# Performance work log

Measured on AMD Instinct MI355X. Metric: run time of the kernel, lower is better.

## Reference

```python
import jax, jax.numpy as jnp
import numpy as np

N_NODES = 50000
N_EDGES = 800000
F_NODE = 64
F_EDGE = 64
HIDDEN = 128


def setup_inputs() -> dict:
    key = jax.random.key(0)
    ks = jax.random.split(key, 12)
    glorot = lambda k, shape: jax.random.normal(k, shape, jnp.float32) * (2.0 / (shape[0] + shape[1])) ** 0.5
    return {
        "x": jax.random.normal(ks[0], (N_NODES, F_NODE), jnp.float32),
        "edge_index": jax.random.randint(ks[1], (2, N_EDGES), 0, N_NODES, jnp.int64),
        "edge_attr": jax.random.normal(ks[2], (N_EDGES, F_EDGE), jnp.float32),
        # edge model: MLP(concat(x_src, x_dst, edge_attr)) -> new edge_attr
        "We1": glorot(ks[3], (2 * F_NODE + F_EDGE, HIDDEN)),
        "be1": jnp.zeros((HIDDEN,), jnp.float32),
        "We2": glorot(ks[4], (HIDDEN, F_EDGE)),
        "be2": jnp.zeros((F_EDGE,), jnp.float32),
        # node model: MLP(concat(x, mean_{e: dst==i} edge_attr_e)) -> new x
        "Wn1": glorot(ks[5], (F_NODE + F_EDGE, HIDDEN)),
        "bn1": jnp.zeros((HIDDEN,), jnp.float32),
        "Wn2": glorot(ks[6], (HIDDEN, F_NODE)),
        "bn2": jnp.zeros((F_NODE,), jnp.float32),
    }


def _mlp(h, W1, b1, W2, b2):
    return jax.nn.relu(h @ W1 + b1) @ W2 + b2


def reference(x, edge_index, edge_attr, We1, be1, We2, be2, Wn1, bn1, Wn2, bn2):
    row, col = edge_index[0], edge_index[1]
    # edge model: message on each edge  [E, 2F+Fe] -> [E, Fe]
    edge_in = jnp.concatenate([x[row], x[col], edge_attr], axis=-1)
    edge_attr = _mlp(edge_in, We1, be1, We2, be2)
    # node model: mean-aggregate incoming messages at dst (col), then MLP
    agg = jax.ops.segment_sum(edge_attr, col, num_segments=N_NODES)
    cnt = jax.ops.segment_sum(jnp.ones((edge_attr.shape[0],), x.dtype), col, num_segments=N_NODES)
    agg = agg / jnp.maximum(cnt, 1.0)[:, None]
    node_in = jnp.concatenate([x, agg], axis=-1)
    x = _mlp(node_in, Wn1, bn1, Wn2, bn2)
    return (x, edge_attr)
```

## Files before the change

kernel.cpp:

```cpp
#include <hip/hip_runtime.h>


typedef __attribute__((ext_vector_type(8))) short bf16x8;
typedef __attribute__((ext_vector_type(4))) float f4;
typedef __attribute__((ext_vector_type(8))) unsigned short us8;

constexpr int NN  = 50000;
constexpr int NE  = 800000;
constexpr int FN  = 64;
constexpr int FE  = 64;
constexpr int HID = 128;
constexpr int K1  = 2 * FN + FE;
constexpr int K2  = FN + FE;
constexpr int GRID_E    = 2500;
constexpr int TPB_TILES = 5;
constexpr int ZAGG_TOT = NN * FE / 8;
constexpr int PACK_TOT = 7168;
constexpr int XCVT_TOT = NN * FN / 8;
constexpr int PREP_TOT = ZAGG_TOT + PACK_TOT + XCVT_TOT + NE;

__device__ __forceinline__ float b2f(unsigned short u) {
  union { unsigned int i; float f; } v; v.i = ((unsigned int)u) << 16; return v.f;
}
__device__ __forceinline__ unsigned short f2b(float f) {
  union { float f; unsigned int i; } v; v.f = f;
  unsigned int r = v.i + 0x7FFFu + ((v.i >> 16) & 1u);
  return (unsigned short)(r >> 16);
}
__device__ __forceinline__ void st16(const f4* r, unsigned short* dst) {
  us8 o0, o1;
#pragma unroll
  for (int j = 0; j < 4; j++) {
    o0[j] = f2b(r[0][j]); o0[4 + j] = f2b(r[1][j]);
    o1[j] = f2b(r[2][j]); o1[4 + j] = f2b(r[3][j]);
  }
  *(us8*)dst = o0; *(us8*)(dst + 8) = o1;
}
__device__ __forceinline__ void ld16(const float* p, f4* r) {
  const f4* pp = (const f4*)p;
  r[0] = pp[0]; r[1] = pp[1]; r[2] = pp[2]; r[3] = pp[3];
}
__device__ __forceinline__ f4 MF(bf16x8 a, bf16x8 b, f4 c) {
  return __builtin_amdgcn_mfma_f32_16x16x32_bf16(a, b, c, 0, 0, 0);
}
__device__ __forceinline__ void pk_atomic_add_bf16(unsigned short* addr, unsigned int data) {
  asm volatile("global_atomic_pk_add_bf16 %0, %1, off" :: "v"(addr), "v"(data) : "memory");
}

__global__ void zero_cnt_kernel(float* __restrict__ cnt) {
  int i = blockIdx.x * 256 + threadIdx.x;
  if (i < NN) cnt[i] = 0.f;
}

__global__ void prep_kernel(const float* __restrict__ We1, const float* __restrict__ We2,
                            const float* __restrict__ Wn1, const float* __restrict__ Wn2,
                            const float* __restrict__ x, const int* __restrict__ ei,
                            unsigned short* __restrict__ P, unsigned short* __restrict__ xb,
                            unsigned short* __restrict__ aggb, float* __restrict__ cnt) {
  int idx = blockIdx.x * 256 + threadIdx.x;
  if (idx < ZAGG_TOT) {
    *(us8*)(aggb + (size_t)idx * 8) = (us8)0;
  } else if (idx < ZAGG_TOT + PACK_TOT) {
    int w = idx - ZAGG_TOT;
    const float* W; unsigned short* Pd; int N;
    if (w < 3072)      { W = We1; Pd = P; N = HID; }
    else if (w < 4096) { W = We2; Pd = P + 24576; N = FE;  w -= 3072; }
    else if (w < 6144) { W = Wn1; Pd = P + 32768; N = HID; w -= 4096; }
    else               { W = Wn2; Pd = P + 49152; N = FN;  w -= 6144; }
    const int l  = w & 63;
    const int nt = (w >> 6) % (N >> 4);
    const int s  = w / ((N >> 4) << 6);
    const int col = nt * 16 + (l & 15);
    const int k0  = s * 32 + (l >> 4) * 8;
    us8 o;
#pragma unroll
    for (int j = 0; j < 8; j++) o[j] = f2b(W[(size_t)(k0 + j) * N + col]);
    *(us8*)(Pd + (size_t)w * 8) = o;
  } else if (idx < ZAGG_TOT + PACK_TOT + XCVT_TOT) {
    const int i = idx - ZAGG_TOT - PACK_TOT;
    const f4* p = (const f4*)(x + (size_t)i * 8);
    f4 a = p[0], b = p[1];
    us8 o;
#pragma unroll
    for (int j = 0; j < 4; j++) { o[j] = f2b(a[j]); o[4 + j] = f2b(b[j]); }
    *(us8*)(xb + (size_t)i * 8) = o;
  } else if (idx < PREP_TOT) {
    const int e = idx - ZAGG_TOT - PACK_TOT - XCVT_TOT;
    atomicAdd(&cnt[ei[NE + e]], 1.0f);
  }
}

__global__ __launch_bounds__(256) void edge_mlp(
    const unsigned short* __restrict__ xb, const int* __restrict__ ei,
    const float* __restrict__ ea,
    const unsigned short* __restrict__ P1, const float* __restrict__ be1,
    const unsigned short* __restrict__ P2, const float* __restrict__ be2,
    float* __restrict__ eout, unsigned short* __restrict__ aggb) {
  __shared__ unsigned short sA[2][64][200];
  __shared__ unsigned short sH[64][136];
  __shared__ int sC[2][64];
  const int tid  = threadIdx.x;
  const int wave = tid >> 6, lane = tid & 63;
  const int mrow = lane & 15, kq = lane >> 4;
  const int el = tid >> 2, q = tid & 3;

  us8 rx0[2], rx1[2];
  f4  rea[4];
  int rN, cN;
  int cStage;

  {
    const int ge = blockIdx.x * 64 + el;
    const int r = ei[ge], c = ei[NE + ge];
    cStage = c;
    const us8* pr = (const us8*)(xb + (size_t)r * FN + q * 16);
    rx0[0] = pr[0]; rx0[1] = pr[1];
    const us8* pc = (const us8*)(xb + (size_t)c * FN + q * 16);
    rx1[0] = pc[0]; rx1[1] = pc[1];
    ld16(ea + (size_t)ge * FE + q * 16, rea);
    const int ge1 = (blockIdx.x + GRID_E) * 64 + el;
    rN = ei[ge1];
    cN = ei[NE + ge1];
    sC[0][el] = cStage;
    *(us8*)&sA[0][el][q * 16]          = rx0[0];
    *(us8*)&sA[0][el][q * 16 + 8]      = rx0[1];
    *(us8*)&sA[0][el][64 + q * 16]     = rx1[0];
    *(us8*)&sA[0][el][64 + q * 16 + 8] = rx1[1];
    st16(rea, &sA[0][el][128 + q * 16]);
  }

  for (int j = 0; j < TPB_TILES; j++) {
    const int cur = j & 1, nxt = cur ^ 1;
    const int e0 = (blockIdx.x + j * GRID_E) * 64;
    __syncthreads();

    if (j + 1 < TPB_TILES) {
      const int rr = rN, cc = cN;
      cStage = cc;
      const int geN = e0 + GRID_E * 64 + el;
      const us8* pr = (const us8*)(xb + (size_t)rr * FN + q * 16);
      rx0[0] = pr[0]; rx0[1] = pr[1];
      const us8* pc = (const us8*)(xb + (size_t)cc * FN + q * 16);
      rx1[0] = pc[0]; rx1[1] = pc[1];
      ld16(ea + (size_t)geN * FE + q * 16, rea);
      if (j + 2 < TPB_TILES) {
        const int ge2 = e0 + 2 * GRID_E * 64 + el;
        rN = ei[ge2];
        cN = ei[NE + ge2];
      }
    }
    __builtin_amdgcn_sched_barrier(0);

    f4 acc[4][2];
#pragma unroll
    for (int m = 0; m < 4; m++) { acc[m][0] = (f4)0.f; acc[m][1] = (f4)0.f; }
    const int nt0 = wave * 2;
#pragma unroll
    for (int s = 0; s < 6; s++) {
      bf16x8 b0 = *(const bf16x8*)(P1 + (((size_t)s * 8 + nt0)     * 64 + lane) * 8);
      bf16x8 b1 = *(const bf16x8*)(P1 + (((size_t)s * 8 + nt0 + 1) * 64 + lane) * 8);
#pragma unroll
      for (int m = 0; m < 4; m++) {
        bf16x8 a = *(const bf16x8*)&sA[cur][m * 16 + mrow][s * 32 + kq * 8];
        acc[m][0] = MF(a, b0, acc[m][0]);
        acc[m][1] = MF(a, b1, acc[m][1]);
      }
    }

    {
      const int c0 = nt0 * 16 + mrow, c1 = c0 + 16;
      const float bb0 = be1[c0], bb1 = be1[c1];
      const int rb = kq * 4;
#pragma unroll
      for (int m = 0; m < 4; m++)
#pragma unroll
        for (int i = 0; i < 4; i++) {
          sH[m * 16 + rb + i][c0] = f2b(fmaxf(acc[m][0][i] + bb0, 0.f));
          sH[m * 16 + rb + i][c1] = f2b(fmaxf(acc[m][1][i] + bb1, 0.f));
        }
    }
    __syncthreads();

    f4 a2[4];
#pragma unroll
    for (int m = 0; m < 4; m++) a2[m] = (f4)0.f;
#pragma unroll
    for (int s = 0; s < 4; s++) {
      bf16x8 b = *(const bf16x8*)(P2 + (((size_t)s * 4 + wave) * 64 + lane) * 8);
#pragma unroll
      for (int m = 0; m < 4; m++) {
        bf16x8 a = *(const bf16x8*)&sH[m * 16 + mrow][s * 32 + kq * 8];
        a2[m] = MF(a, b, a2[m]);
      }
    }

    {
      const int col = wave * 16 + mrow;
      const float bb = be2[col];
      const int rb = kq * 4;
      const bool even = ((lane & 1) == 0);
#pragma unroll
      for (int m = 0; m < 4; m++)
#pragma unroll
        for (int i = 0; i < 4; i++) {
          const int er = m * 16 + rb + i;
          const float v = a2[m][i] + bb;
          eout[(size_t)(e0 + er) * FE + col] = v;
          const float vp = __shfl_xor(v, 1);
          if (even) {
            const unsigned int pk =
                (unsigned int)f2b(v) | ((unsigned int)f2b(vp) << 16);
            pk_atomic_add_bf16(aggb + ((size_t)sC[cur][er] * FE + col), pk);
          }
        }
    }

    if (j + 1 < TPB_TILES) {
      sC[nxt][el] = cStage;
      *(us8*)&sA[nxt][el][q * 16]          = rx0[0];
      *(us8*)&sA[nxt][el][q * 16 + 8]      = rx0[1];
      *(us8*)&sA[nxt][el][64 + q * 16]     = rx1[0];
      *(us8*)&sA[nxt][el][64 + q * 16 + 8] = rx1[1];
      st16(rea, &sA[nxt][el][128 + q * 16]);
    }
  }
}

__global__ __launch_bounds__(256) void node_mlp(
    const unsigned short* __restrict__ xb, const unsigned short* __restrict__ aggb,
    const float* __restrict__ cnt,
    const unsigned short* __restrict__ P1, const float* __restrict__ bn1,
    const unsigned short* __restrict__ P2, const float* __restrict__ bn2,
    float* __restrict__ xout) {
  __shared__ unsigned short sA[32][136];
  unsigned short (*sH)[136] = (unsigned short(*)[136])&sA[0][0];
  const int tid = threadIdx.x;
  const int n0  = blockIdx.x * 32;

  {
    const int nl = tid >> 3, q = tid & 7;
    const int gn = n0 + nl;
    if (gn < NN) {
      if (q < 4) {
        const us8* p = (const us8*)(xb + (size_t)gn * FN + q * 16);
        *(us8*)&sA[nl][q * 16]     = p[0];
        *(us8*)&sA[nl][q * 16 + 8] = p[1];
      } else {
        const float inv = 1.0f / fmaxf(cnt[gn], 1.0f);
        const int q4 = q - 4;
        const us8* pa = (const us8*)(aggb + (size_t)gn * FE + q4 * 16);
#pragma unroll
        for (int seg = 0; seg < 2; seg++) {
          us8 a = pa[seg];
          us8 o;
#pragma unroll
          for (int jj = 0; jj < 8; jj++) o[jj] = f2b(b2f(a[jj]) * inv);
          *(us8*)&sA[nl][64 + q4 * 16 + seg * 8] = o;
        }
      }
    } else {
      us8 z = (us8)0;
      *(us8*)&sA[nl][(q & 3) * 16]     = z;
      *(us8*)&sA[nl][(q & 3) * 16 + 8] = z;
      *(us8*)&sA[nl][64 + (q & 3) * 16]     = z;
      *(us8*)&sA[nl][64 + (q & 3) * 16 + 8] = z;
    }
  }
  __syncthreads();

  const int wave = tid >> 6, lane = tid & 63;
  const int mrow = lane & 15, kq = lane >> 4;

  f4 acc[2][2];
#pragma unroll
  for (int m = 0; m < 2; m++) { acc[m][0] = (f4)0.f; acc[m][1] = (f4)0.f; }
  const int nt0 = wave * 2;
#pragma unroll
  for (int s = 0; s < 4; s++) {
    bf16x8 b0 = *(const bf16x8*)(P1 + (((size_t)s * 8 + nt0)     * 64 + lane) * 8);
    bf16x8 b1 = *(const bf16x8*)(P1 + (((size_t)s * 8 + nt0 + 1) * 64 + lane) * 8);
#pragma unroll
    for (int m = 0; m < 2; m++) {
      bf16x8 a = *(const bf16x8*)&sA[m * 16 + mrow][s * 32 + kq * 8];
      acc[m][0] = MF(a, b0, acc[m][0]);
      acc[m][1] = MF(a, b1, acc[m][1]);
    }
  }
  __syncthreads();

  {
    const int c0 = nt0 * 16 + mrow, c1 = c0 + 16;
    const float bb0 = bn1[c0], bb1 = bn1[c1];
    const int rb = kq * 4;
#pragma unroll
    for (int m = 0; m < 2; m++)
#pragma unroll
      for (int i = 0; i < 4; i++) {
        sH[m * 16 + rb + i][c0] = f2b(fmaxf(acc[m][0][i] + bb0, 0.f));
        sH[m * 16 + rb + i][c1] = f2b(fmaxf(acc[m][1][i] + bb1, 0.f));
      }
  }
  __syncthreads();

  f4 a2[2];
  a2[0] = (f4)0.f; a2[1] = (f4)0.f;
#pragma unroll
  for (int s = 0; s < 4; s++) {
    bf16x8 b = *(const bf16x8*)(P2 + (((size_t)s * 4 + wave) * 64 + lane) * 8);
#pragma unroll
    for (int m = 0; m < 2; m++) {
      bf16x8 a = *(const bf16x8*)&sH[m * 16 + mrow][s * 32 + kq * 8];
      a2[m] = MF(a, b, a2[m]);
    }
  }
  {
    const int col = wave * 16 + mrow;
    const float bb = bn2[col];
    const int rb = kq * 4;
#pragma unroll
    for (int m = 0; m < 2; m++)
#pragma unroll
      for (int i = 0; i < 4; i++) {
        const int gn = n0 + m * 16 + rb + i;
        if (gn < NN) xout[(size_t)gn * FN + col] = a2[m][i] + bb;
      }
  }
}

extern "C" void kernel_launch(void* const* d_in, const int* in_sizes, int n_in,
                              void* d_out, int out_size, void* d_ws, size_t ws_size,
                              hipStream_t stream) {
  if (n_in != 11) return;
  if (in_sizes[0] != NN * FN) return;
  if (in_sizes[1] != 2 * NE) return;
  if (in_sizes[2] != NE * FE) return;
  if (out_size != NN * FN + NE * FE) return;
  if (ws_size < (size_t)NN * FE * 2 + (size_t)NN * 4 + 114688 + (size_t)NN * FN * 2) return;

  const float* x   = (const float*)d_in[0];
  const int*   ei  = (const int*)d_in[1];
  const float* ea  = (const float*)d_in[2];
  const float* We1 = (const float*)d_in[3];
  const float* be1 = (const float*)d_in[4];
  const float* We2 = (const float*)d_in[5];
  const float* be2 = (const float*)d_in[6];
  const float* Wn1 = (const float*)d_in[7];
  const float* bn1 = (const float*)d_in[8];
  const float* Wn2 = (const float*)d_in[9];
  const float* bn2 = (const float*)d_in[10];

  float* xout = (float*)d_out;
  float* eout = xout + (size_t)NN * FN;

  unsigned short* aggb = (unsigned short*)d_ws;
  float* cnt = (float*)(aggb + (size_t)NN * FE);
  unsigned short* P  = (unsigned short*)(cnt + NN);
  unsigned short* Pe1 = P;
  unsigned short* Pe2 = P + 24576;
  unsigned short* Pn1 = P + 32768;
  unsigned short* Pn2 = P + 49152;
  unsigned short* xb  = P + 57344;

  zero_cnt_kernel<<<(NN + 255) / 256, 256, 0, stream>>>(cnt);
  prep_kernel<<<(PREP_TOT + 255) / 256, 256, 0, stream>>>(
      We1, We2, Wn1, Wn2, x, ei, P, xb, aggb, cnt);
  edge_mlp<<<GRID_E, 256, 0, stream>>>(xb, ei, ea, Pe1, be1, Pe2, be2, eout, aggb);
  node_mlp<<<(NN + 31) / 32, 256, 0, stream>>>(xb, aggb, cnt, Pn1, bn1, Pn2, bn2, xout);
}
```

Baseline: 263.8 us.

## Fold count zeroing into prep and move degree counting into edge kernel blocks

Removes the separate zero-count kernel by zeroing the count buffer inside the prep kernel with vector stores. The per-edge degree atomics move out of prep into extra blocks appended to the edge MLP grid, where they run alongside the MLP tiles. This saves one launch and shortens the prep kernel's critical path. The extra blocks add atomic traffic inside the edge kernel and take the same large shared-memory allocation, which may reduce occupancy for the MLP blocks.

```diff
diff --git a/kernel.cpp b/kernel.cpp
--- a/kernel.cpp
+++ b/kernel.cpp
@@ -13,11 +13,13 @@
 constexpr int K1  = 2 * FN + FE;
 constexpr int K2  = FN + FE;
 constexpr int GRID_E    = 2500;
+constexpr int CNT_BLK   = 512;
 constexpr int TPB_TILES = 5;
 constexpr int ZAGG_TOT = NN * FE / 8;
+constexpr int ZCNT_TOT = NN / 4;
 constexpr int PACK_TOT = 7168;
 constexpr int XCVT_TOT = NN * FN / 8;
-constexpr int PREP_TOT = ZAGG_TOT + PACK_TOT + XCVT_TOT + NE;
+constexpr int PREP_TOT = ZAGG_TOT + ZCNT_TOT + PACK_TOT + XCVT_TOT;
 
 __device__ __forceinline__ float b2f(unsigned short u) {
   union { unsigned int i; float f; } v; v.i = ((unsigned int)u) << 16; return v.f;
@@ -47,21 +49,19 @@
   asm volatile("global_atomic_pk_add_bf16 %0, %1, off" :: "v"(addr), "v"(data) : "memory");
 }
 
-__global__ void zero_cnt_kernel(float* __restrict__ cnt) {
-  int i = blockIdx.x * 256 + threadIdx.x;
-  if (i < NN) cnt[i] = 0.f;
-}
-
 __global__ void prep_kernel(const float* __restrict__ We1, const float* __restrict__ We2,
                             const float* __restrict__ Wn1, const float* __restrict__ Wn2,
-                            const float* __restrict__ x, const int* __restrict__ ei,
+                            const float* __restrict__ x,
                             unsigned short* __restrict__ P, unsigned short* __restrict__ xb,
                             unsigned short* __restrict__ aggb, float* __restrict__ cnt) {
   int idx = blockIdx.x * 256 + threadIdx.x;
   if (idx < ZAGG_TOT) {
     *(us8*)(aggb + (size_t)idx * 8) = (us8)0;
-  } else if (idx < ZAGG_TOT + PACK_TOT) {
-    int w = idx - ZAGG_TOT;
+  } else if (idx < ZAGG_TOT + ZCNT_TOT) {
+    const int i = idx - ZAGG_TOT;
+    *(f4*)(cnt + (size_t)i * 4) = (f4)0.f;
+  } else if (idx < ZAGG_TOT + ZCNT_TOT + PACK_TOT) {
+    int w = idx - ZAGG_TOT - ZCNT_TOT;
     const float* W; unsigned short* Pd; int N;
     if (w < 3072)      { W = We1; Pd = P; N = HID; }
     else if (w < 4096) { W = We2; Pd = P + 24576; N = FE;  w -= 3072; }
@@ -76,17 +76,14 @@
 #pragma unroll
     for (int j = 0; j < 8; j++) o[j] = f2b(W[(size_t)(k0 + j) * N + col]);
     *(us8*)(Pd + (size_t)w * 8) = o;
-  } else if (idx < ZAGG_TOT + PACK_TOT + XCVT_TOT) {
-    const int i = idx - ZAGG_TOT - PACK_TOT;
+  } else if (idx < PREP_TOT) {
+    const int i = idx - ZAGG_TOT - ZCNT_TOT - PACK_TOT;
     const f4* p = (const f4*)(x + (size_t)i * 8);
     f4 a = p[0], b = p[1];
     us8 o;
 #pragma unroll
     for (int j = 0; j < 4; j++) { o[j] = f2b(a[j]); o[4 + j] = f2b(b[j]); }
     *(us8*)(xb + (size_t)i * 8) = o;
-  } else if (idx < PREP_TOT) {
-    const int e = idx - ZAGG_TOT - PACK_TOT - XCVT_TOT;
-    atomicAdd(&cnt[ei[NE + e]], 1.0f);
   }
 }
 
@@ -95,7 +92,15 @@
     const float* __restrict__ ea,
     const unsigned short* __restrict__ P1, const float* __restrict__ be1,
     const unsigned short* __restrict__ P2, const float* __restrict__ be2,
-    float* __restrict__ eout, unsigned short* __restrict__ aggb) {
+    float* __restrict__ eout, unsigned short* __restrict__ aggb,
+    float* __restrict__ cnt) {
+  if (blockIdx.x >= GRID_E) {
+    int t = (blockIdx.x - GRID_E) * 256 + threadIdx.x;
+    for (int e = t; e < NE; e += CNT_BLK * 256)
+      atomicAdd(&cnt[ei[NE + e]], 1.0f);
+    return;
+  }
+
   __shared__ unsigned short sA[2][64][200];
   __shared__ unsigned short sH[64][136];
   __shared__ int sC[2][64];
@@ -361,9 +366,9 @@
   unsigned short* Pn2 = P + 49152;
   unsigned short* xb  = P + 57344;
 
-  zero_cnt_kernel<<<(NN + 255) / 256, 256, 0, stream>>>(cnt);
   prep_kernel<<<(PREP_TOT + 255) / 256, 256, 0, stream>>>(
-      We1, We2, Wn1, Wn2, x, ei, P, xb, aggb, cnt);
-  edge_mlp<<<GRID_E, 256, 0, stream>>>(xb, ei, ea, Pe1, be1, Pe2, be2, eout, aggb);
+      We1, We2, Wn1, Wn2, x, P, xb, aggb, cnt);
+  edge_mlp<<<GRID_E + CNT_BLK, 256, 0, stream>>>(
+      xb, ei, ea, Pe1, be1, Pe2, be2, eout, aggb, cnt);
   node_mlp<<<(NN + 31) / 32, 256, 0, stream>>>(xb, aggb, cnt, Pn1, bn1, Pn2, bn2, xout);
 }
```

Result: faster. 253.7 us (-3.8%).
